# Kernel tuning notes

Hardware: AMD Instinct MI355X
Metric: run time of the kernel (lower is better)

Reference implementation:

```python
import jax, jax.numpy as jnp
import numpy as np

B, N, RD = 32, 2000, 32
E, H, A = 128, 256, 8
NUM_ACTIONS = N
ACTION_NORM = float(NUM_ACTIONS)


def _mlp2(x, W1, b1, W2, b2):
    return jnp.maximum(x @ W1 + b1, 0.0) @ W2 + b2


def setup_inputs() -> dict:
    key = jax.random.key(0)
    ks = jax.random.split(key, 8)
    s = lambda fan_in: 1.0 / np.sqrt(fan_in)
    return {
        "state": jax.random.normal(ks[0], (B, N, RD), jnp.float32),
        "distance_matrix": jax.random.uniform(ks[1], (N, N), jnp.float32),
        "W_emb1": jax.random.normal(ks[2], (RD, H), jnp.float32) * s(RD),
        "b_emb1": jnp.zeros((H,), jnp.float32),
        "W_emb2": jax.random.normal(ks[3], (H, E), jnp.float32) * s(H),
        "b_emb2": jnp.zeros((E,), jnp.float32),
        "Wq1": jax.random.normal(ks[4], (E + A, H), jnp.float32) * s(E + A),
        "bq1": jnp.zeros((H,), jnp.float32),
        "Wq2": jax.random.normal(ks[5], (H, 1), jnp.float32) * s(H),
        "bq2": jnp.zeros((1,), jnp.float32),
        "fixed_actions": jax.random.randint(ks[6], (3, B), 0, NUM_ACTIONS, jnp.int32),
        "fixed_agent_ids": jnp.arange(3, dtype=jnp.int32),
    }


def reference(state, distance_matrix, W_emb1, b_emb1, W_emb2, b_emb2,
              Wq1, bq1, Wq2, bq2, fixed_actions, fixed_agent_ids):
    # normalized distance -> similarity, row-stochastic
    dm = distance_matrix / distance_matrix.max()
    sim = jnp.exp(-dm)  # scaling = 1 (use_nn_scaling=False)
    sim = sim / sim.sum(-1, keepdims=True)

    enc = _mlp2(state, W_emb1, b_emb1, W_emb2, b_emb2)      # [B,N,E]
    x = jnp.einsum('nm,bme->bne', sim, enc)                 # graph conv mix

    idx_f = jnp.arange(N, dtype=x.dtype)

    def qnet(actions):
        # actions: [B,A] broadcast over node axis -> concat -> MLP -> [B,N]
        act = jnp.broadcast_to(actions[:, None, :], (B, N, A))
        feat = jnp.concatenate([x, act], axis=-1)           # [B,N,E+A]
        return _mlp2(feat, Wq1, bq1, Wq2, bq2)[..., 0]      # [B,N]

    # init actions: -1 everywhere, fixed agents get given action / norm
    actions = jnp.full((B, A), -1.0, dtype=x.dtype)
    actions = actions.at[:, fixed_agent_ids].set(
        fixed_actions.T.astype(x.dtype) / ACTION_NORM)

    # sequential per-agent soft-argmax loop (second torch loop; the first
    # torch loop's q-values are fully overwritten here, so it is dead code)
    q_cols = []
    for agent_id in range(A):
        q = qnet(actions)                                   # [B,N]
        sam = jnp.clip(jax.nn.softmax(q, axis=-1) @ idx_f, 0.0, float(NUM_ACTIONS))
        actions = actions.at[:, agent_id].set(
            jax.lax.stop_gradient(sam / ACTION_NORM))
        q2 = qnet(actions)
        qv = jnp.take_along_axis(q2, sam.astype(jnp.int32)[:, None], axis=-1)[:, 0]
        q_cols.append(qv)

    q_values = jnp.stack(q_cols, axis=1)                    # [B,A]
    chosen = (actions * ACTION_NORM).astype(jnp.int32)      # [B,A]
    return q_values, chosen
```

## Files before the change

kernel.cpp:

```cpp
#include <hip/hip_runtime.h>
#include <cstddef>

#define NB 32
#define NN 2000
#define NRD 32
#define NE 128
#define NH 256
#define NA 8
#define KP8 2048
#define NGP 128
#define H1S 264
#define XT8S 136
#define ACTION_NORM 2000.0f

typedef unsigned short u16;
typedef unsigned char u8;
typedef __bf16 b16x8 __attribute__((ext_vector_type(8)));
typedef float f32x4 __attribute__((ext_vector_type(4)));
typedef const __attribute__((address_space(1))) unsigned int* gptr_t;
typedef __attribute__((address_space(3))) unsigned int* lptr_t;

__device__ inline u16 f2bf(float x) {
    unsigned u = __float_as_uint(x);
    u += 0x7FFFu + ((u >> 16) & 1u);
    return (u16)(u >> 16);
}
__device__ inline float bf2f(u16 h) { return __uint_as_float((unsigned)h << 16); }
__device__ inline u8 f2fp8(float x) {
    return (u8)(__builtin_amdgcn_cvt_pk_fp8_f32(x, x, 0, false) & 0xFF);
}
__device__ inline u16 f2fp8x2(float a, float b) {
    return (u16)(__builtin_amdgcn_cvt_pk_fp8_f32(a, b, 0, false) & 0xFFFF);
}
__device__ inline float fp82f(u8 b) {
    return __builtin_amdgcn_cvt_pk_f32_fp8((unsigned)b, false)[0];
}
__device__ inline int kswz(int m) {
    return (m & ~63) + (((m >> 3) & 3) << 4) + (((m >> 5) & 1) << 3) + (m & 7);
}

#define PREP_STATE (64000 * 32)
#define PREP_W1T   (256 * 32)
#define PREP_W2T   (128 * 256)
#define PREP_WQ1T  (256 * 128)
#define PREP_PAD   (4096 * 48)
#define PREP_TOT   (PREP_STATE + PREP_W1T + PREP_W2T + PREP_WQ1T + PREP_PAD)
#define PREP_BLOCKS (PREP_TOT / 256)
#define MAX_BLOCKS 1024
__global__ __launch_bounds__(256) void k_front(
        const float* __restrict__ state, const float* __restrict__ W1,
        const float* __restrict__ W2, const float* __restrict__ Wq1,
        const float* __restrict__ dm, const int* __restrict__ fa,
        const int* __restrict__ fid,
        u16* __restrict__ state_b, u16* __restrict__ W1t,
        u16* __restrict__ W2t, u8* __restrict__ Wq1f8,
        u8* __restrict__ encb, float* __restrict__ pmax,
        float* __restrict__ actions, float* __restrict__ ap0,
        float2* __restrict__ part0) {
    __shared__ float sh[256];
    const int blk = blockIdx.x, t = threadIdx.x;
    if (blk < PREP_BLOCKS) {
        int i = blk * 256 + t;
        if (i < PREP_STATE) { state_b[i] = f2bf(state[i]); return; }
        i -= PREP_STATE;
        if (i < PREP_W1T) { int h = i >> 5, k = i & 31; W1t[i] = f2bf(W1[k * NH + h]); return; }
        i -= PREP_W1T;
        if (i < PREP_W2T) { int e = i >> 8, h = i & 255; W2t[i] = f2bf(W2[h * NE + e]); return; }
        i -= PREP_W2T;
        if (i < PREP_WQ1T) { int hq = i >> 7, e = i & 127; Wq1f8[i] = f2fp8(Wq1[e * NH + hq]); return; }
        i -= PREP_WQ1T;
        if (i < PREP_PAD) { int eb = i / 48, mm = NN + (i % 48); encb[(size_t)eb * KP8 + kswz(mm)] = 0; }
        return;
    }
    if (blk < PREP_BLOCKS + MAX_BLOCKS) {
        const int bid = blk - PREP_BLOCKS;
        float m = 0.0f;
        for (size_t i = (size_t)bid * 256 + t; i < (size_t)NN * NN; i += (size_t)MAX_BLOCKS * 256)
            m = fmaxf(m, dm[i]);
        sh[t] = m; __syncthreads();
        for (int s = 128; s > 0; s >>= 1) {
            if (t < s) sh[t] = fmaxf(sh[t], sh[t + s]);
            __syncthreads();
        }
        if (t == 0) pmax[bid] = sh[0];
        return;
    }
    const int b = t >> 3, a = t & 7;
    float v = -1.0f;
    for (int j = 0; j < 3; ++j)
        if (fid[j] == a) v = (float)fa[j * NB + b] / ACTION_NORM;
    actions[t] = v;
    sh[t] = v;
    __syncthreads();
    float wq[NA];
#pragma unroll
    for (int aa = 0; aa < NA; ++aa) wq[aa] = Wq1[(size_t)(NE + aa) * NH + t];
    for (int bb = 0; bb < NB; ++bb) {
        float s = 0.0f;
#pragma unroll
        for (int aa = 0; aa < NA; ++aa) s = fmaf(sh[bb * NA + aa], wq[aa], s);
        ap0[bb * NH + t] = s;
    }
    for (int i = t; i < NB * NGP; i += 256) part0[i] = make_float2(0.0f, 0.0f);
}

__global__ __launch_bounds__(512) void k_sim_enc(
        const u16* __restrict__ state_b, const u16* __restrict__ W1t,
        const u16* __restrict__ W2t, u8* __restrict__ encb,
        const float* __restrict__ b1, const float* __restrict__ b2,
        const float* __restrict__ dm, const float* __restrict__ pmax,
        u8* __restrict__ simb, float* __restrict__ inv_rs) {
    __shared__ u16 stage[20 * 512];
    __shared__ u16 h1t[64 * H1S];
    const int blk = blockIdx.x, tid = threadIdx.x;

    if (blk >= 1000) {
        float* shf = (float*)stage;
        const int n = blk - 1000, t = tid;
        float m = fmaxf(pmax[t], pmax[t + 512]);
        shf[t] = m; __syncthreads();
        for (int s = 256; s > 0; s >>= 1) {
            if (t < s) shf[t] = fmaxf(shf[t], shf[t + s]);
            __syncthreads();
        }
        const float inv = 1.0f / shf[0];
        __syncthreads();
        float s = 0.0f;
        for (int mm = t * 2; mm < KP8; mm += 1024) {
            float e0 = 0.0f, e1 = 0.0f;
            if (mm < NN)     { e0 = expf(-dm[(size_t)n * NN + mm] * inv);     s += e0; }
            if (mm + 1 < NN) { e1 = expf(-dm[(size_t)n * NN + mm + 1] * inv); s += e1; }
            *(u16*)(simb + (size_t)n * KP8 + kswz(mm)) = f2fp8x2(e0, e1);
        }
        shf[t] = s; __syncthreads();
        for (int st = 256; st > 0; st >>= 1) {
            if (t < st) shf[t] += shf[t + st];
            __syncthreads();
        }
        if (t == 0) inv_rs[n] = 1.0f / shf[0];
        return;
    }

    const int w = tid >> 6, l = tid & 63;
    const int lm = l & 15, lq = l >> 4;
    const int gm = blk * 64;

    {
#pragma unroll
        for (int i = 0; i < 3; ++i) {
            const int idx = w * 3 + i;
            if (idx < 20) {
                const u16* gp;
                if (idx < 4) gp = state_b + (size_t)(gm + idx * 16 + lm) * NRD + lq * 8;
                else         gp = W1t + (size_t)((idx - 4) * 16 + lm) * NRD + lq * 8;
                __builtin_amdgcn_global_load_lds((gptr_t)gp, (lptr_t)(stage + idx * 512), 16, 0, 0);
            }
        }
        __syncthreads();
        b16x8 af[4], bf[2];
#pragma unroll
        for (int i = 0; i < 4; ++i) af[i] = *(const b16x8*)(stage + i * 512 + l * 8);
#pragma unroll
        for (int j = 0; j < 2; ++j) bf[j] = *(const b16x8*)(stage + (4 + w * 2 + j) * 512 + l * 8);
        f32x4 acc1[4][2] = {};
#pragma unroll
        for (int i = 0; i < 4; ++i)
#pragma unroll
            for (int j = 0; j < 2; ++j)
                acc1[i][j] = __builtin_amdgcn_mfma_f32_16x16x32_bf16(af[i], bf[j], acc1[i][j], 0, 0, 0);
#pragma unroll
        for (int i = 0; i < 4; ++i)
#pragma unroll
            for (int r = 0; r < 4; ++r) {
                const int row = i * 16 + lq * 4 + r;
#pragma unroll
                for (int j = 0; j < 2; ++j) {
                    const int col = w * 32 + j * 16 + lm;
                    h1t[row * H1S + col] = f2bf(fmaxf(acc1[i][j][r] + b1[col], 0.0f));
                }
            }
    }

    const int wr = w & 3, wc = w >> 2;
    f32x4 acc2[2][2] = {};
    const u16* gpw = W2t + (size_t)(w * 16 + lm) * NH + lq * 8;
    __syncthreads();
    __builtin_amdgcn_global_load_lds((gptr_t)gpw, (lptr_t)(stage + w * 512), 16, 0, 0);
    __syncthreads();
    for (int t = 0; t < 8; ++t) {
        const int cur = t & 1;
        if (t < 7) {
            gpw += 32;
            __builtin_amdgcn_global_load_lds((gptr_t)gpw,
                (lptr_t)(stage + (cur ^ 1) * 4096 + w * 512), 16, 0, 0);
        }
        const u16* base = stage + cur * 4096;
        b16x8 af2[2], bf2[2];
#pragma unroll
        for (int i = 0; i < 2; ++i)
            af2[i] = *(const b16x8*)(base + (wr * 2 + i) * 512 + l * 8);
#pragma unroll
        for (int j = 0; j < 2; ++j)
            bf2[j] = *(const b16x8*)(h1t + (wc * 32 + j * 16 + lm) * H1S + t * 32 + lq * 8);
#pragma unroll
        for (int i = 0; i < 2; ++i)
#pragma unroll
            for (int j = 0; j < 2; ++j)
                acc2[i][j] = __builtin_amdgcn_mfma_f32_16x16x32_bf16(af2[i], bf2[j], acc2[i][j], 0, 0, 0);
        __syncthreads();
    }
#pragma unroll
    for (int i = 0; i < 2; ++i)
#pragma unroll
        for (int r = 0; r < 4; ++r) {
            const int e = wr * 32 + i * 16 + lq * 4 + r;
            const float bias = b2[e];
#pragma unroll
            for (int j = 0; j < 2; ++j) {
                const int rg = gm + wc * 32 + j * 16 + lm;
                const unsigned bb = (unsigned)rg / 2000u;
                const unsigned mm = (unsigned)rg - bb * 2000u;
                encb[((size_t)bb * 128 + e) * KP8 + kswz((int)mm)] = f2fp8(acc2[i][j][r] + bias);
            }
        }
}

__global__ __launch_bounds__(512) void k_conv_y0(
        const u8* __restrict__ simb, const u8* __restrict__ encb,
        const u8* __restrict__ Wq1f8, const float* __restrict__ inv_rs,
        const float* __restrict__ bq1, const float* __restrict__ ap0,
        const float* __restrict__ Wq2, u8* __restrict__ y0f8,
        float2* __restrict__ part0) {
    __shared__ u8 lds[2 * 16 * 1024];
    __shared__ u8 xt8[128 * XT8S];
    __shared__ float qsum[64 * 8];
    const int tid = threadIdx.x;
    const int w = tid >> 6, l = tid & 63;
    const int wr = w & 1, wc = w >> 1;
    const int bm = blockIdx.x * 128;
    const int bb = blockIdx.y;
    const int lm = l & 15, lq = l >> 4;
    const u8* Bt = encb + (size_t)bb * 128 * KP8;
    typedef long lx2 __attribute__((ext_vector_type(2)));

    f32x4 acc[4][2] = {};

    const u8* gpt[2];
#pragma unroll
    for (int i = 0; i < 2; ++i) {
        const int idx = w * 2 + i;
        if (idx < 8) {
            int row = bm + idx * 16 + lm;
            row = row < NN ? row : NN - 1;
            gpt[i] = simb + (size_t)row * KP8 + lq * 16;
        } else {
            gpt[i] = Bt + (size_t)((idx - 8) * 16 + lm) * KP8 + lq * 16;
        }
    }
#pragma unroll
    for (int i = 0; i < 2; ++i)
        __builtin_amdgcn_global_load_lds((gptr_t)gpt[i],
            (lptr_t)(lds + (w * 2 + i) * 1024), 16, 0, 0);
    __syncthreads();

    for (int t = 0; t < KP8 / 64; ++t) {
        const u8* curb = lds + (t & 1) * 16384;
        if (t < KP8 / 64 - 1) {
            u8* nxtb = lds + ((t + 1) & 1) * 16384;
#pragma unroll
            for (int i = 0; i < 2; ++i) {
                gpt[i] += 64;
                __builtin_amdgcn_global_load_lds((gptr_t)gpt[i],
                    (lptr_t)(nxtb + (w * 2 + i) * 1024), 16, 0, 0);
            }
        }
        const int fo = l * 16;
        lx2 af[4], bf[2];
#pragma unroll
        for (int i = 0; i < 4; ++i)
            af[i] = *(const lx2*)(curb + (wr * 4 + i) * 1024 + fo);
#pragma unroll
        for (int j = 0; j < 2; ++j)
            bf[j] = *(const lx2*)(curb + (8 + wc * 2 + j) * 1024 + fo);
#pragma unroll
        for (int i = 0; i < 4; ++i)
#pragma unroll
            for (int j = 0; j < 2; ++j) {
                acc[i][j] = __builtin_amdgcn_mfma_f32_16x16x32_fp8_fp8(af[i][0], bf[j][0], acc[i][j], 0, 0, 0);
                acc[i][j] = __builtin_amdgcn_mfma_f32_16x16x32_fp8_fp8(af[i][1], bf[j][1], acc[i][j], 0, 0, 0);
            }
        __syncthreads();
    }

#pragma unroll
    for (int i = 0; i < 4; ++i) {
#pragma unroll
        for (int r = 0; r < 4; ++r) {
            const int row = wr * 64 + i * 16 + lq * 4 + r;
            const int gn = bm + row;
            const float rsv = inv_rs[gn < NN ? gn : NN - 1];
#pragma unroll
            for (int j = 0; j < 2; ++j) {
                const int col = wc * 32 + j * 16 + lm;
                xt8[row * XT8S + col] = f2fp8(acc[i][j][r] * rsv);
            }
        }
    }
    __syncthreads();

    const int h0 = w * 32;
    float bq1v[2], apv[2], w2vv[2];
#pragma unroll
    for (int j = 0; j < 2; ++j) {
        const int h = h0 + j * 16 + lm;
        bq1v[j] = bq1[h];
        apv[j] = ap0[bb * NH + h];
        w2vv[j] = Wq2[h];
    }
    float se_tot = 0.0f, sn_tot = 0.0f;

    for (int half = 0; half < 2; ++half) {
        f32x4 acc2[4][2] = {};
#pragma unroll
        for (int ks = 0; ks < 4; ++ks) {
            long bfw[2];
#pragma unroll
            for (int j = 0; j < 2; ++j)
                bfw[j] = *(const long*)(Wq1f8 + (size_t)(h0 + j * 16 + lm) * NE + ks * 32 + lq * 8);
#pragma unroll
            for (int i = 0; i < 4; ++i) {
                const long afx = *(const long*)(xt8 + (half * 64 + i * 16 + lm) * XT8S + ks * 32 + lq * 8);
#pragma unroll
                for (int j = 0; j < 2; ++j)
                    acc2[i][j] = __builtin_amdgcn_mfma_f32_16x16x32_fp8_fp8(afx, bfw[j], acc2[i][j], 0, 0, 0);
            }
        }
#pragma unroll
        for (int i = 0; i < 4; ++i) {
#pragma unroll
            for (int r = 0; r < 4; ++r) {
                const int rl = i * 16 + lq * 4 + r;
                const int n = bm + half * 64 + rl;
                float q = 0.0f;
#pragma unroll
                for (int j = 0; j < 2; ++j) {
                    const float v = acc2[i][j][r] + bq1v[j];
                    if (n < NN) y0f8[((size_t)n * NB + bb) * NH + h0 + j * 16 + lm] = f2fp8(v);
                    q += fmaxf(v + apv[j], 0.0f) * w2vv[j];
                }
#pragma unroll
                for (int off = 1; off < 16; off <<= 1) q += __shfl_xor(q, off);
                if (lm == 0) qsum[rl * 8 + w] = q;
            }
        }
        __syncthreads();
        if (tid < 64) {
            const int n = bm + half * 64 + tid;
            float q = 0.0f;
#pragma unroll
            for (int wv = 0; wv < 8; ++wv) q += qsum[tid * 8 + wv];
            float e = (n < NN) ? expf(fminf(q, 60.0f)) : 0.0f;
            float sne = e * (float)n;
#pragma unroll
            for (int off = 32; off > 0; off >>= 1) {
                e += __shfl_xor(e, off); sne += __shfl_xor(sne, off);
            }
            if (tid == 0) { se_tot += e; sn_tot += sne; }
        }
        __syncthreads();
    }
    if (tid == 0) part0[bb * NGP + blockIdx.x] = make_float2(se_tot, sn_tot);
}

__global__ __launch_bounds__(256) void k_agent(
        const u8* __restrict__ y0f8, const float* __restrict__ Wq1,
        const float* __restrict__ Wq2, const float* __restrict__ bq2,
        float* actions, const float2* __restrict__ pin, float2* __restrict__ pout,
        float* __restrict__ out, int ag) {
    __shared__ float sh[256];
    __shared__ float s_sam;
    const int t = threadIdx.x;
    const int lane = t & 63, wave = t >> 6;
    const int wg = blockIdx.x * 4 + wave;
    const int b = wg & 31, ng = wg >> 5;
    const int hl = lane & 15, qtr = lane >> 4;

    float act[NA];
#pragma unroll
    for (int a = 0; a < NA; ++a) act[a] = actions[b * NA + a];
    {
        const float2 p0 = pin[b * NGP + lane];
        const float2 p1 = pin[b * NGP + 64 + lane];
        float se0 = p0.x + p1.x, sn0 = p0.y + p1.y;
#pragma unroll
        for (int m = 32; m > 0; m >>= 1) {
            se0 += __shfl_xor(se0, m); sn0 += __shfl_xor(sn0, m);
        }
        const float sam = fminf(fmaxf(sn0 / se0, 0.0f), 2000.0f);
        act[ag - 1] = sam * (1.0f / ACTION_NORM);
    }
    float ap16[16] = {};
#pragma unroll
    for (int a = 0; a < NA; ++a) {
        const float av = act[a];
        const float4* wq = (const float4*)(Wq1 + (size_t)(NE + a) * NH + hl * 16);
#pragma unroll
        for (int jj = 0; jj < 4; ++jj) {
            const float4 w4 = wq[jj];
            ap16[jj * 4 + 0] = fmaf(av, w4.x, ap16[jj * 4 + 0]);
            ap16[jj * 4 + 1] = fmaf(av, w4.y, ap16[jj * 4 + 1]);
            ap16[jj * 4 + 2] = fmaf(av, w4.z, ap16[jj * 4 + 2]);
            ap16[jj * 4 + 3] = fmaf(av, w4.w, ap16[jj * 4 + 3]);
        }
    }
    float w2v[16];
    {
        const float4* w2p = (const float4*)(Wq2 + hl * 16);
#pragma unroll
        for (int jj = 0; jj < 4; ++jj) {
            const float4 w4 = w2p[jj];
            w2v[jj * 4 + 0] = w4.x; w2v[jj * 4 + 1] = w4.y;
            w2v[jj * 4 + 2] = w4.z; w2v[jj * 4 + 3] = w4.w;
        }
    }

    float se = 0.0f, sn = 0.0f;
#pragma unroll
    for (int k = 0; k < 4; ++k) {
        const int p = ng + k * NGP;
        if (p >= NN / 4) break;
        const int n = 4 * p + qtr;
        const uint4 yv = *(const uint4*)(y0f8 + (((size_t)n * NB + b) << 8) + hl * 16);
        const unsigned dw[4] = {yv.x, yv.y, yv.z, yv.w};
        float q = 0.0f;
#pragma unroll
        for (int d = 0; d < 4; ++d) {
            const auto lo = __builtin_amdgcn_cvt_pk_f32_fp8(dw[d], false);
            const auto hi = __builtin_amdgcn_cvt_pk_f32_fp8(dw[d], true);
            q += fmaxf(lo[0] + ap16[d * 4 + 0], 0.f) * w2v[d * 4 + 0];
            q += fmaxf(lo[1] + ap16[d * 4 + 1], 0.f) * w2v[d * 4 + 1];
            q += fmaxf(hi[0] + ap16[d * 4 + 2], 0.f) * w2v[d * 4 + 2];
            q += fmaxf(hi[1] + ap16[d * 4 + 3], 0.f) * w2v[d * 4 + 3];
        }
#pragma unroll
        for (int off = 1; off < 16; off <<= 1) q += __shfl_xor(q, off);
        const float e = expf(fminf(q, 60.0f));
        se += e; sn += e * (float)n;
    }
    se += __shfl_xor(se, 16); sn += __shfl_xor(sn, 16);
    se += __shfl_xor(se, 32); sn += __shfl_xor(sn, 32);
    if (lane == 0) pout[b * NGP + ng] = make_float2(se, sn);

    if (blockIdx.x < NB) {
        const int bb = blockIdx.x;
        if (wave == 0) {
            const float2 p0 = pin[bb * NGP + lane];
            const float2 p1 = pin[bb * NGP + 64 + lane];
            float a1 = p0.x + p1.x, a2 = p0.y + p1.y;
#pragma unroll
            for (int m = 32; m > 0; m >>= 1) {
                a1 += __shfl_xor(a1, m); a2 += __shfl_xor(a2, m);
            }
            if (lane == 0) s_sam = fminf(fmaxf(a2 / a1, 0.0f), 2000.0f);
        }
        __syncthreads();
        const float sam = s_sam;
        const float samn = sam * (1.0f / ACTION_NORM);
        float apt = 0.0f;
#pragma unroll
        for (int a = 0; a < NA; ++a) {
            const float av = (a == ag - 1) ? samn : actions[bb * NA + a];
            apt = fmaf(av, Wq1[(size_t)(NE + a) * NH + t], apt);
        }
        int nsel = (int)sam; if (nsel > NN - 1) nsel = NN - 1;
        const float yv = fp82f(y0f8[((size_t)nsel * NB + bb) * NH + t]);
        sh[t] = fmaxf(yv + apt, 0.0f) * Wq2[t];
        __syncthreads();
        for (int s = 128; s > 0; s >>= 1) {
            if (t < s) sh[t] += sh[t + s];
            __syncthreads();
        }
        if (t == 0) {
            out[bb * NA + (ag - 1)] = sh[0] + bq2[0];
            actions[bb * NA + (ag - 1)] = samn;
        }
    }
}

__global__ __launch_bounds__(256) void k_fin(
        const u8* __restrict__ y0f8, const float* __restrict__ Wq1,
        const float* __restrict__ Wq2, const float* __restrict__ bq2,
        const float* __restrict__ actions, const float2* __restrict__ pin,
        float* __restrict__ out) {
    __shared__ float sh[256];
    __shared__ float s_sam;
    const int bb = blockIdx.x, t = threadIdx.x;
    const int lane = t & 63, wave = t >> 6;
    if (wave == 0) {
        const float2 p0 = pin[bb * NGP + lane];
        const float2 p1 = pin[bb * NGP + 64 + lane];
        float a1 = p0.x + p1.x, a2 = p0.y + p1.y;
#pragma unroll
        for (int m = 32; m > 0; m >>= 1) {
            a1 += __shfl_xor(a1, m); a2 += __shfl_xor(a2, m);
        }
        if (lane == 0) s_sam = fminf(fmaxf(a2 / a1, 0.0f), 2000.0f);
    }
    __syncthreads();
    const float sam = s_sam;
    const float samn = sam * (1.0f / ACTION_NORM);
    float apt = 0.0f;
#pragma unroll
    for (int a = 0; a < NA; ++a) {
        const float av = (a == NA - 1) ? samn : actions[bb * NA + a];
        apt = fmaf(av, Wq1[(size_t)(NE + a) * NH + t], apt);
    }
    int nsel = (int)sam; if (nsel > NN - 1) nsel = NN - 1;
    const float yv = fp82f(y0f8[((size_t)nsel * NB + bb) * NH + t]);
    sh[t] = fmaxf(yv + apt, 0.0f) * Wq2[t];
    __syncthreads();
    for (int s = 128; s > 0; s >>= 1) {
        if (t < s) sh[t] += sh[t + s];
        __syncthreads();
    }
    if (t == 0) out[bb * NA + (NA - 1)] = sh[0] + bq2[0];
    if (t < NA) {
        const float av = (t == NA - 1) ? samn : actions[bb * NA + t];
        out[NB * NA + bb * NA + t] = (float)(int)(av * ACTION_NORM);
    }
}

extern "C" void kernel_launch(void* const* d_in, const int* in_sizes, int n_in,
                              void* d_out, int out_size, void* d_ws, size_t ws_size,
                              hipStream_t stream) {
    const float* state = (const float*)d_in[0];
    const float* dm    = (const float*)d_in[1];
    const float* W1    = (const float*)d_in[2];
    const float* b1    = (const float*)d_in[3];
    const float* W2    = (const float*)d_in[4];
    const float* b2    = (const float*)d_in[5];
    const float* Wq1   = (const float*)d_in[6];
    const float* bq1   = (const float*)d_in[7];
    const float* Wq2   = (const float*)d_in[8];
    const float* bq2   = (const float*)d_in[9];
    const int* fa      = (const int*)d_in[10];
    const int* fid     = (const int*)d_in[11];
    float* out = (float*)d_out;

    char* p = (char*)d_ws;
    u8* simb       = (u8*)p;       p += (size_t)NN * KP8;
    u8* encb       = (u8*)p;       p += (size_t)4096 * KP8;
    float* inv_rs  = (float*)p;    p += 2048 * 4;
    float* pmax    = (float*)p;    p += 1024 * 4;
    float* actions = (float*)p;    p += 256 * 4;
    float* ap0     = (float*)p;    p += 8192 * 4;
    float2* part0  = (float2*)p;   p += (size_t)NB * NGP * 8;
    float2* part1  = (float2*)p;   p += (size_t)NB * NGP * 8;
    u16* state_b   = (u16*)p;      p += (size_t)2048000 * 2;
    u16* W1t       = (u16*)p;      p += 8192 * 2;
    u16* W2t       = (u16*)p;      p += 32768 * 2;
    u8* Wq1f8      = (u8*)p;       p += 32768;
    u8* y0f8       = (u8*)p;       p += (size_t)16384000;

    k_front<<<PREP_BLOCKS + MAX_BLOCKS + 1, 256, 0, stream>>>(
        state, W1, W2, Wq1, dm, fa, fid,
        state_b, W1t, W2t, Wq1f8, encb, pmax, actions, ap0, part0);
    k_sim_enc<<<3000, 512, 0, stream>>>(state_b, W1t, W2t, encb, b1, b2,
                                        dm, pmax, simb, inv_rs);
    k_conv_y0<<<dim3(16, 32), 512, 0, stream>>>(simb, encb, Wq1f8, inv_rs, bq1,
                                                ap0, Wq2, y0f8, part0);
    for (int ag = 1; ag < NA; ++ag) {
        const float2* pin  = (ag & 1) ? part0 : part1;
        float2*       pout = (ag & 1) ? part1 : part0;
        k_agent<<<1024, 256, 0, stream>>>(y0f8, Wq1, Wq2, bq2, actions,
                                          pin, pout, out, ag);
    }
    k_fin<<<NB, 256, 0, stream>>>(y0f8, Wq1, Wq2, bq2, actions, part1, out);
}
```

Before: 262.3 us.

## Triple-buffer conv GEMM K-loop with explicit vmcnt barriers and MFMA priority

Changes the fp8 sim×enc GEMM in k_conv_y0 from a double-buffered loop to a three-stage ring buffer. Loads are issued two tiles ahead, and the loop waits on vmcnt before each barrier instead of draining every load. MFMA sections are raised in priority with s_setprio, and the xt8 staging buffer now aliases the ring buffer so LDS use stays roughly the same. The goal is to hide global-to-LDS latency better, at the cost of hand-tuned waitcnt counts that must match the number of outstanding loads.

```diff
diff --git a/kernel.cpp b/kernel.cpp
--- a/kernel.cpp
+++ b/kernel.cpp
@@ -231,8 +231,7 @@
         const float* __restrict__ bq1, const float* __restrict__ ap0,
         const float* __restrict__ Wq2, u8* __restrict__ y0f8,
         float2* __restrict__ part0) {
-    __shared__ u8 lds[2 * 16 * 1024];
-    __shared__ u8 xt8[128 * XT8S];
+    __shared__ u8 lds[3 * 16384];
     __shared__ float qsum[64 * 8];
     const int tid = threadIdx.x;
     const int w = tid >> 6, l = tid & 63;
@@ -257,23 +256,15 @@
             gpt[i] = Bt + (size_t)((idx - 8) * 16 + lm) * KP8 + lq * 16;
         }
     }
-#pragma unroll
-    for (int i = 0; i < 2; ++i)
-        __builtin_amdgcn_global_load_lds((gptr_t)gpt[i],
-            (lptr_t)(lds + (w * 2 + i) * 1024), 16, 0, 0);
-    __syncthreads();
-
-    for (int t = 0; t < KP8 / 64; ++t) {
-        const u8* curb = lds + (t & 1) * 16384;
-        if (t < KP8 / 64 - 1) {
-            u8* nxtb = lds + ((t + 1) & 1) * 16384;
-#pragma unroll
-            for (int i = 0; i < 2; ++i) {
-                gpt[i] += 64;
-                __builtin_amdgcn_global_load_lds((gptr_t)gpt[i],
-                    (lptr_t)(nxtb + (w * 2 + i) * 1024), 16, 0, 0);
-            }
-        }
+
+    auto STAGE = [&](int kt, int buf) {
+#pragma unroll
+        for (int i = 0; i < 2; ++i)
+            __builtin_amdgcn_global_load_lds((gptr_t)(gpt[i] + kt * 64),
+                (lptr_t)(lds + buf * 16384 + (w * 2 + i) * 1024), 16, 0, 0);
+    };
+    auto COMPUTE = [&](int buf) {
+        const u8* curb = lds + buf * 16384;
         const int fo = l * 16;
         lx2 af[4], bf[2];
 #pragma unroll
@@ -282,6 +273,7 @@
 #pragma unroll
         for (int j = 0; j < 2; ++j)
             bf[j] = *(const lx2*)(curb + (8 + wc * 2 + j) * 1024 + fo);
+        __builtin_amdgcn_s_setprio(1);
 #pragma unroll
         for (int i = 0; i < 4; ++i)
 #pragma unroll
@@ -289,8 +281,32 @@
                 acc[i][j] = __builtin_amdgcn_mfma_f32_16x16x32_fp8_fp8(af[i][0], bf[j][0], acc[i][j], 0, 0, 0);
                 acc[i][j] = __builtin_amdgcn_mfma_f32_16x16x32_fp8_fp8(af[i][1], bf[j][1], acc[i][j], 0, 0, 0);
             }
-        __syncthreads();
-    }
+        __builtin_amdgcn_s_setprio(0);
+    };
+
+#define FENCE() __builtin_amdgcn_sched_barrier(0)
+#define BAR_BARE() do { FENCE(); asm volatile("" ::: "memory"); \
+    __builtin_amdgcn_s_barrier(); FENCE(); } while (0)
+#define BAR_VM(N) do { FENCE(); asm volatile("s_waitcnt vmcnt(" #N ")" ::: "memory"); \
+    __builtin_amdgcn_s_barrier(); FENCE(); } while (0)
+
+    STAGE(0, 0);
+    STAGE(1, 1);
+    for (int t = 0; t < 30; ++t) {
+        STAGE(t + 2, (t + 2) % 3);
+        BAR_VM(4);
+        COMPUTE(t % 3);
+        BAR_BARE();
+    }
+    BAR_VM(2);
+    COMPUTE(0);
+    BAR_BARE();
+    BAR_VM(0);
+    COMPUTE(1);
+    BAR_BARE();
+#undef BAR_VM
+#undef BAR_BARE
+#undef FENCE
 
 #pragma unroll
     for (int i = 0; i < 4; ++i) {
@@ -302,7 +318,7 @@
 #pragma unroll
             for (int j = 0; j < 2; ++j) {
                 const int col = wc * 32 + j * 16 + lm;
-                xt8[row * XT8S + col] = f2fp8(acc[i][j][r] * rsv);
+                lds[row * XT8S + col] = f2fp8(acc[i][j][r] * rsv);
             }
         }
     }
@@ -329,7 +345,7 @@
                 bfw[j] = *(const long*)(Wq1f8 + (size_t)(h0 + j * 16 + lm) * NE + ks * 32 + lq * 8);
 #pragma unroll
             for (int i = 0; i < 4; ++i) {
-                const long afx = *(const long*)(xt8 + (half * 64 + i * 16 + lm) * XT8S + ks * 32 + lq * 8);
+                const long afx = *(const long*)(lds + (half * 64 + i * 16 + lm) * XT8S + ks * 32 + lq * 8);
 #pragma unroll
                 for (int j = 0; j < 2; ++j)
                     acc2[i][j] = __builtin_amdgcn_mfma_f32_16x16x32_fp8_fp8(afx, bfw[j], acc2[i][j], 0, 0, 0);
```

Result: no change. 260.0 us (-0.9%).
